# Optimization experiments

Hardware: AMD Instinct MI355X
Metric: run time of the kernel (lower is better)

The kernel has to match this reference:

```python
import jax, jax.numpy as jnp
import numpy as np

B = 64      # num graphs
NPG = 800   # nodes per graph
N = B * NPG
EPG = 6400  # edges per graph (avg degree 8)
APG = 64    # feasible actions per graph
H = 4       # attention heads
C = 64      # hidden channels per head
OUT = 128   # out_channels


def _gat_params(key, fin, h, c, concat):
    k1, k2, k3 = jax.random.split(key, 3)
    s = 1.0 / np.sqrt(fin)
    W = jax.random.uniform(k1, (fin, h * c), jnp.float32, -s, s)
    a_src = jax.random.uniform(k2, (h, c), jnp.float32, -s, s)
    a_dst = jax.random.uniform(k3, (h, c), jnp.float32, -s, s)
    b = jnp.zeros((h * c if concat else c,), jnp.float32)
    return W, a_src, a_dst, b


def _lin_params(key, fin, fout):
    k1, k2 = jax.random.split(key)
    s = 1.0 / np.sqrt(fin)
    W = jax.random.uniform(k1, (fin, fout), jnp.float32, -s, s)
    b = jax.random.uniform(k2, (fout,), jnp.float32, -s, s)
    return W, b


def setup_inputs() -> dict:
    key = jax.random.key(0)
    ks = list(jax.random.split(key, 24))
    x = jax.random.normal(ks[0], (N, 5), jnp.float32)
    offs = jnp.arange(B, dtype=jnp.int32) * NPG
    src = jax.random.randint(ks[1], (B, EPG), 0, NPG, jnp.int32) + offs[:, None]
    dst = jax.random.randint(ks[2], (B, EPG), 0, NPG, jnp.int32) + offs[:, None]
    edge_index = jnp.stack([src.reshape(-1), dst.reshape(-1)])
    batch = jnp.repeat(jnp.arange(B, dtype=jnp.int32), NPG)
    actions_idx = (jax.random.randint(ks[3], (B, APG, 2), 0, NPG, jnp.int32)
                   + offs[:, None, None]).reshape(-1, 2)
    tabu_label = (jax.random.uniform(ks[4], (B * APG, 1)) < 0.5).astype(jnp.float32)
    inp = dict(x=x, edge_index=edge_index, batch=batch,
               actions_idx=actions_idx, tabu_label=tabu_label)
    names = ['f1', 'f2', 'f3', 'b1', 'b2', 'b3']
    fins = [3, H * C, H * C, 3, H * C, H * C]
    hs = [H, H, 1, H, H, 1]
    cs = [C, C, OUT, C, C, OUT]
    concats = [True, True, False, True, True, False]
    for i, nm in enumerate(names):
        W, a_s, a_d, b = _gat_params(ks[5 + i], fins[i], hs[i], cs[i], concats[i])
        inp[nm + '_W'] = W; inp[nm + '_as'] = a_s; inp[nm + '_ad'] = a_d; inp[nm + '_b'] = b
    dims = [(8 * OUT + 1, 2 * OUT), (2 * OUT, 2 * OUT), (2 * OUT, 2 * OUT), (2 * OUT, 1)]
    for i, (fi, fo) in enumerate(dims):
        W, b = _lin_params(ks[12 + i], fi, fo)
        inp['p_W%d' % (i + 1)] = W; inp['p_b%d' % (i + 1)] = b
    return inp


def _gat(h, s, d, W, a_src, a_dst, bias, concat):
    # PyG GATConv: project, per-edge attention, softmax over target index, scatter-add
    n = h.shape[0]
    Hh, Cc = a_src.shape
    xp = (h @ W).reshape(n, Hh, Cc)                      # [N,H,C]
    al_s = (xp * a_src).sum(-1)                          # [N,H]
    al_d = (xp * a_dst).sum(-1)                          # [N,H]
    e = jax.nn.leaky_relu(al_s[s] + al_d[d], 0.2)        # [E,H]
    m = jax.ops.segment_max(e, d, num_segments=n)
    ex = jnp.exp(e - m[d])
    den = jax.ops.segment_sum(ex, d, num_segments=n)
    alpha = ex / (den[d] + 1e-16)
    out = jax.ops.segment_sum(xp[s] * alpha[..., None], d, num_segments=n)  # [N,H,C]
    out = out.reshape(n, Hh * Cc) if concat else out.mean(axis=1)
    return out + bias


def reference(x, edge_index, batch, actions_idx, tabu_label,
              f1_W, f1_as, f1_ad, f1_b, f2_W, f2_as, f2_ad, f2_b,
              f3_W, f3_as, f3_ad, f3_b, b1_W, b1_as, b1_ad, b1_b,
              b2_W, b2_as, b2_ad, b2_b, b3_W, b3_as, b3_ad, b3_b,
              p_W1, p_b1, p_W2, p_b2, p_W3, p_b3, p_W4, p_b4):
    n = x.shape[0]
    ar = jnp.arange(n, dtype=edge_index.dtype)
    ei = jnp.concatenate([edge_index, jnp.stack([ar, ar])], axis=1)  # add_self_loops
    src, dst = ei[0], ei[1]
    # forward branch (flow source_to_target)
    hf = x[:, jnp.array([0, 1, 3])]
    hf = jax.nn.elu(_gat(hf, src, dst, f1_W, f1_as, f1_ad, f1_b, True))
    hf = jax.nn.elu(_gat(hf, src, dst, f2_W, f2_as, f2_ad, f2_b, True))
    hf3 = _gat(hf, src, dst, f3_W, f3_as, f3_ad, f3_b, False)
    # backward branch (flow target_to_source == reversed edges)
    hb = x[:, jnp.array([0, 2, 4])]
    hb = jax.nn.elu(_gat(hb, dst, src, b1_W, b1_as, b1_ad, b1_b, True))
    hb = jax.nn.elu(_gat(hb, dst, src, b2_W, b2_as, b2_ad, b2_b, True))
    hb3 = _gat(hb, dst, src, b3_W, b3_as, b3_ad, b3_b, False)
    h_node = jnp.concatenate([hf3, hb3], axis=-1)        # [N, 2*OUT]
    counts = jax.ops.segment_sum(jnp.ones((n,), x.dtype), batch, num_segments=B)
    g_pool = jax.ops.segment_sum(h_node, batch, num_segments=B) / counts[:, None]
    node_h = jnp.concatenate([h_node, g_pool[batch]], axis=-1)  # [N, 4*OUT]
    action_h = jnp.concatenate([node_h[actions_idx[:, 0]],
                                node_h[actions_idx[:, 1]],
                                tabu_label], axis=-1)    # [A, 8*OUT+1]
    h = jnp.tanh(action_h @ p_W1 + p_b1)
    h = jnp.tanh(h @ p_W2 + p_b2)
    h = jnp.tanh(h @ p_W3 + p_b3)
    score = (h @ p_W4 + p_b4).reshape(B, APG)
    log_prob = jax.nn.log_softmax(score, axis=-1)        # [B, APG]
    entropy = -(jnp.exp(log_prob) * log_prob).sum(-1, keepdims=True)  # [B,1]
    return (log_prob, entropy)
```

## Files before the change

### kernel.cpp

```cpp
#include <hip/hip_runtime.h>
#include <hip/hip_bf16.h>
#include <math.h>

constexpr int NN  = 51200;
constexpr int EE  = 409600;
constexpr int BB  = 64;
constexpr int APG = 64;
constexpr int NPG = 800;
constexpr int SCAN_N = 2 * NN;
constexpr int NA = BB * APG;
constexpr int KF = 1056;

typedef __bf16 bf16x8 __attribute__((ext_vector_type(8)));
typedef float f32x4 __attribute__((ext_vector_type(4)));
typedef float f32x2 __attribute__((ext_vector_type(2)));
typedef __attribute__((address_space(1))) const void g_void;
typedef __attribute__((address_space(3))) void l_void;

__device__ __forceinline__ float leaky(float x) { return fmaxf(x, 0.2f * x); }
__device__ __forceinline__ float bflo(unsigned w) { return __uint_as_float(w << 16); }
__device__ __forceinline__ float bfhi(unsigned w) { return __uint_as_float(w & 0xffff0000u); }
__device__ __forceinline__ unsigned short f2b(float x) {
  __hip_bfloat16 h = __float2bfloat16(x);
  unsigned short u;
  __builtin_memcpy(&u, &h, 2);
  return u;
}
__device__ __forceinline__ unsigned pack2(float a, float b) {
  return (unsigned)f2b(a) | ((unsigned)f2b(b) << 16);
}

__global__ void count_kernel(const int* __restrict__ ei, int* cnt) {
  int e = blockIdx.x * blockDim.x + threadIdx.x;
  if (e >= EE) return;
  int s = ei[e], d = ei[EE + e];
  atomicAdd(&cnt[d], 1);
  atomicAdd(&cnt[NN + s], 1);
}

__global__ __launch_bounds__(256) void scan1_kernel(const int* __restrict__ cnt,
                                                    int* __restrict__ rp,
                                                    int* __restrict__ bsum) {
  __shared__ int wsum[4];
  int b = blockIdx.x, t = threadIdx.x;
  int base = b * 1024 + t * 4;
  int4 v = *(const int4*)(cnt + base);
  int s = v.x + v.y + v.z + v.w;
  int lane = t & 63, wv = t >> 6;
  int incl = s;
  for (int off = 1; off < 64; off <<= 1) {
    int u = __shfl_up(incl, off);
    if (lane >= off) incl += u;
  }
  if (lane == 63) wsum[wv] = incl;
  __syncthreads();
  int woff = 0;
  for (int i = 0; i < wv; i++) woff += wsum[i];
  int excl = woff + incl - s;
  rp[base] = excl;
  rp[base + 1] = excl + v.x;
  rp[base + 2] = excl + v.x + v.y;
  rp[base + 3] = excl + v.x + v.y + v.z;
  if (t == 255) bsum[b] = woff + incl;
}

__global__ void scan2_kernel(const int* __restrict__ bsum, int* __restrict__ boff,
                             int* __restrict__ rp) {
  __shared__ int w0;
  int t = threadIdx.x;
  int v = (t < 100) ? bsum[t] : 0;
  int lane = t & 63;
  int incl = v;
  for (int off = 1; off < 64; off <<= 1) {
    int u = __shfl_up(incl, off);
    if (lane >= off) incl += u;
  }
  if (t == 63) w0 = incl;
  __syncthreads();
  int excl = incl - v + ((t >= 64) ? w0 : 0);
  if (t < 100) boff[t] = excl;
  if (t == 99) rp[SCAN_N] = excl + v;
}

__global__ __launch_bounds__(256) void scan3_kernel(int* __restrict__ rp,
                                                    const int* __restrict__ boff) {
  int b = blockIdx.x;
  int off = boff[b];
  int i = b * 1024 + threadIdx.x * 4;
  int4 v = *(int4*)(rp + i);
  v.x += off; v.y += off; v.z += off; v.w += off;
  *(int4*)(rp + i) = v;
}

__global__ void fill_kernel(const int* __restrict__ ei, const int* __restrict__ rp,
                            int* pos, int* __restrict__ col) {
  int e = blockIdx.x * blockDim.x + threadIdx.x;
  if (e >= EE) return;
  int s = ei[e], d = ei[EE + e];
  int p = atomicAdd(&pos[d], 1);
  col[rp[d] + p] = s;
  int q = atomicAdd(&pos[NN + s], 1);
  col[rp[NN + s] + q] = d;
}

__global__ __launch_bounds__(256) void precomp_kernel(const float* __restrict__ Wf,
                                                      const float* __restrict__ Wb,
                                                      const float* __restrict__ asf,
                                                      const float* __restrict__ adf,
                                                      const float* __restrict__ asb,
                                                      const float* __restrict__ adb,
                                                      float* __restrict__ wa) {
  int wave = (blockIdx.x * blockDim.x + threadIdx.x) >> 6;
  int lane = threadIdx.x & 63;
  if (wave >= 48) return;
  int dir = wave / 24, sd = (wave / 12) % 2, h = (wave / 3) % 4, c = wave % 3;
  const float* W = dir ? Wb : Wf;
  const float* a = dir ? (sd ? adb : asb) : (sd ? adf : asf);
  float v = W[c * 256 + h * 64 + lane] * a[h * 64 + lane];
  for (int off = 1; off < 64; off <<= 1) v += __shfl_xor(v, off);
  if (lane == 0) wa[wave] = v;
}

__global__ __launch_bounds__(256) void lin1_kernel(const float* __restrict__ x,
                                                   const float* __restrict__ Wf,
                                                   const float* __restrict__ Wb,
                                                   const float* __restrict__ wa,
                                                   __hip_bfloat16* __restrict__ out,
                                                   float* __restrict__ al_s,
                                                   float* __restrict__ al_d) {
  int idx = blockIdx.x * 256 + threadIdx.x;
  int n = idx >> 5, grp = idx & 31;
  int dir = (n >= NN) ? 1 : 0;
  int node = dir ? n - NN : n;
  const float* W = dir ? Wb : Wf;
  int c1 = dir ? 2 : 1, c2 = dir ? 4 : 3;
  float f0 = x[node * 5], f1 = x[node * 5 + c1], f2 = x[node * 5 + c2];
  int j0 = grp * 8;
  float v[8];
#pragma unroll
  for (int j = 0; j < 8; j++)
    v[j] = f0 * W[j0 + j] + f1 * W[256 + j0 + j] + f2 * W[512 + j0 + j];
  uint4 u;
  u.x = pack2(v[0], v[1]);
  u.y = pack2(v[2], v[3]);
  u.z = pack2(v[4], v[5]);
  u.w = pack2(v[6], v[7]);
  *(uint4*)(out + (size_t)n * 256 + j0) = u;
  if (grp < 4) {
    const float* ws = wa + dir * 24 + grp * 3;
    const float* wd = wa + dir * 24 + 12 + grp * 3;
    al_s[n * 4 + grp] = f0 * ws[0] + f1 * ws[1] + f2 * ws[2];
    al_d[n * 4 + grp] = f0 * wd[0] + f1 * wd[1] + f2 * wd[2];
  }
}

template <int HH>
__global__ __launch_bounds__(256) void alpha_kernel(const float* __restrict__ als,
                                                    const float* __restrict__ ald,
                                                    const int* __restrict__ rp,
                                                    const int* __restrict__ col,
                                                    float* __restrict__ alpha,
                                                    float* __restrict__ alpha_self) {
  int b = blockIdx.x;
  int xcd = b & 7, q = b >> 3;
  int g2 = (q / 25) * 8 + xcd;
  int d = g2 * 800 + (q % 25) * 32 + (threadIdx.x >> 3);
  int slot = threadIdx.x & 7;
  int off_row = (d >= NN) ? NN : 0;
  float ald_loc[HH], self_w[HH];
#pragma unroll
  for (int h = 0; h < HH; h++) {
    ald_loc[h] = ald[d * HH + h];
    self_w[h] = __expf(leaky(als[d * HH + h] + ald_loc[h]));
  }
  int beg = rp[d], end = rp[d + 1];
  int i0 = beg + slot;
  bool have = i0 < end;
  int s0 = col[have ? i0 : beg] + off_row;
  float sm[HH], w0[HH];
#pragma unroll
  for (int h = 0; h < HH; h++) sm[h] = 0.f;
  if (have) {
#pragma unroll
    for (int h = 0; h < HH; h++) {
      w0[h] = __expf(leaky(als[s0 * HH + h] + ald_loc[h]));
      sm[h] += w0[h];
    }
  }
  for (int i = i0 + 8; i < end; i += 8) {
    int s = col[i] + off_row;
#pragma unroll
    for (int h = 0; h < HH; h++) {
      float w = __expf(leaky(als[s * HH + h] + ald_loc[h]));
      sm[h] += w;
      alpha[(size_t)i * HH + h] = w;
    }
  }
#pragma unroll
  for (int h = 0; h < HH; h++) {
    sm[h] += __shfl_xor(sm[h], 1);
    sm[h] += __shfl_xor(sm[h], 2);
    sm[h] += __shfl_xor(sm[h], 4);
  }
  float inv[HH];
#pragma unroll
  for (int h = 0; h < HH; h++)
    inv[h] = 1.f / (sm[h] + self_w[h] + 1e-16f);
  if (have) {
#pragma unroll
    for (int h = 0; h < HH; h++) alpha[(size_t)i0 * HH + h] = w0[h] * inv[h];
  }
  for (int i = i0 + 8; i < end; i += 8)
#pragma unroll
    for (int h = 0; h < HH; h++) alpha[(size_t)i * HH + h] *= inv[h];
  if (slot == 0) {
#pragma unroll
    for (int h = 0; h < HH; h++)
      alpha_self[d * HH + h] = self_w[h] * inv[h];
  }
}

__device__ __forceinline__ f32x2 unpk(unsigned w) {
  f32x2 v;
  v.x = bflo(w);
  v.y = bfhi(w);
  return v;
}

template <int HH, int CC, int OUT_SPLIT>
__global__ __launch_bounds__(256) void spmm_kernel(const __hip_bfloat16* __restrict__ xp,
                                                   const float* __restrict__ alpha,
                                                   const float* __restrict__ alpha_self,
                                                   const int* __restrict__ rp,
                                                   const int* __restrict__ col,
                                                   const float* __restrict__ biasf,
                                                   const float* __restrict__ biasb,
                                                   __hip_bfloat16* __restrict__ out_bf,
                                                   int do_elu) {
  constexpr int HC = HH * CC;
  constexpr int RDW = HC / 2;
  constexpr int DL = RDW / 32;
  int b = blockIdx.x;
  int xcd = b & 7;
  int bq = b >> 3;
  int dreg = xcd * 12800;
  int t = threadIdx.x;
  int wv = t >> 6, lane = t & 63;
  int sub = lane & 31, halfsel = lane >> 5;
  int lbase = lane & 32;
  int off_row = (dreg >= NN) ? NN : 0;
  const float* bias = (dreg >= NN) ? biasb : biasf;
  int hsel = (HH == 4) ? (sub >> 3) : 0;
  const unsigned* xw = (const unsigned*)xp;
  float bv[2 * DL];
#pragma unroll
  for (int j = 0; j < 2 * DL; j++) bv[j] = bias[sub * 2 * DL + j];

#pragma unroll 1
  for (int it = 0; it < 4; ++it) {
    int d = dreg + it * 3200 + bq * 8 + wv * 2 + halfsel;
    int beg = rp[d];
    int deg = rp[d + 1] - beg;
    int degmax = max(deg, __shfl_xor(deg, 32));
    degmax = __builtin_amdgcn_readfirstlane(degmax);
    float aself = alpha_self[d * HH + hsel];
    f32x2 acc[DL];
    {
      const unsigned* sp = xw + (size_t)d * RDW + sub * DL;
      if constexpr (DL == 4) {
        uint4 sw = *(const uint4*)sp;
        acc[0] = aself * unpk(sw.x);
        acc[1] = aself * unpk(sw.y);
        acc[2] = aself * unpk(sw.z);
        acc[3] = aself * unpk(sw.w);
      } else {
        uint2 sw = *(const uint2*)sp;
        acc[0] = aself * unpk(sw.x);
        acc[1] = aself * unpk(sw.y);
      }
    }
    for (int c0 = 0; c0 < degmax; c0 += 8) {
      int ce = c0 + sub;
      ce = (ce < deg) ? ce : (deg > 0 ? deg - 1 : 0);
      int colv = col[beg + ce];
      colv = ((unsigned)colv < (unsigned)NN) ? colv : 0;
      colv += off_row;
      float av = 0.f;
      if constexpr (HH == 4) {
        int e = c0 + (sub >> 2);
        if (e < deg) av = alpha[(size_t)(beg + e) * 4 + (sub & 3)];
      } else {
        int e = c0 + sub;
        if (e < deg) av = alpha[beg + e];
      }
      uint4 w[8];
#pragma unroll
      for (int k = 0; k < 8; k++) {
        int s = __shfl(colv, lbase + k);
        const unsigned* p = xw + (size_t)s * RDW + sub * DL;
        if constexpr (DL == 4) {
          w[k] = *(const uint4*)p;
        } else {
          uint2 v2 = *(const uint2*)p;
          w[k].x = v2.x;
          w[k].y = v2.y;
        }
      }
#pragma unroll
      for (int k = 0; k < 8; k++) {
        float a;
        if constexpr (HH == 4) a = __shfl(av, lbase + k * 4 + hsel);
        else a = __shfl(av, lbase + k);
        acc[0] += a * unpk(w[k].x);
        acc[1] += a * unpk(w[k].y);
        if constexpr (DL == 4) {
          acc[2] += a * unpk(w[k].z);
          acc[3] += a * unpk(w[k].w);
        }
      }
    }
    float v[2 * DL];
#pragma unroll
    for (int j = 0; j < DL; j++) {
      v[2 * j] = acc[j].x + bv[2 * j];
      v[2 * j + 1] = acc[j].y + bv[2 * j + 1];
    }
    if (do_elu) {
#pragma unroll
      for (int j = 0; j < 2 * DL; j++) v[j] = v[j] > 0.f ? v[j] : (__expf(v[j]) - 1.f);
    }
    if constexpr (OUT_SPLIT) {
      int nd = (d < NN) ? d : d - NN;
      int oo = (d < NN) ? 0 : 64;
      uint2 u;
      u.x = pack2(v[0], v[1]);
      u.y = pack2(v[2], v[3]);
      *(uint2*)((unsigned*)out_bf + (size_t)nd * 128 + oo + sub * 2) = u;
    } else {
      uint4 u;
      u.x = pack2(v[0], v[1]);
      u.y = pack2(v[2], v[3]);
      u.z = pack2(v[4], v[5]);
      u.w = pack2(v[6], v[7]);
      *(uint4*)((unsigned*)out_bf + (size_t)d * RDW + sub * DL) = u;
    }
  }
}

__global__ void castW2_kernel(const float* __restrict__ W0, const float* __restrict__ W1,
                              __hip_bfloat16* __restrict__ Wt0,
                              __hip_bfloat16* __restrict__ Wt1,
                              int K, int N, int Kp) {
  int idx = blockIdx.x * 256 + threadIdx.x;
  int tot = N * Kp;
  if (idx >= 2 * tot) return;
  const float* W = (idx < tot) ? W0 : W1;
  __hip_bfloat16* Wt = (idx < tot) ? Wt0 : Wt1;
  int i = (idx < tot) ? idx : idx - tot;
  int n = i / Kp, k = i % Kp;
  Wt[i] = (k < K) ? __float2bfloat16(W[(size_t)k * N + n]) : __float2bfloat16(0.f);
}

__global__ void castW1_kernel(const float* __restrict__ W, __hip_bfloat16* __restrict__ Wt,
                              int K, int N, int Kp) {
  int idx = blockIdx.x * 256 + threadIdx.x;
  if (idx >= N * Kp) return;
  int n = idx / Kp, k = idx % Kp;
  Wt[idx] = (k < K) ? __float2bfloat16(W[(size_t)k * N + n]) : __float2bfloat16(0.f);
}

template <int EPI, int ALH, int ALCC>
__global__ __launch_bounds__(256) void gemm_mfma(const __hip_bfloat16* __restrict__ A,
                                                 const __hip_bfloat16* __restrict__ Bt0,
                                                 const __hip_bfloat16* __restrict__ Bt1,
                                                 __hip_bfloat16* __restrict__ Cb,
                                                 const float* __restrict__ bias0,
                                                 const float* __restrict__ bias1,
                                                 const float* __restrict__ asv0,
                                                 const float* __restrict__ asv1,
                                                 const float* __restrict__ adv0,
                                                 const float* __restrict__ adv1,
                                                 float* __restrict__ al_s,
                                                 float* __restrict__ al_d,
                                                 int M, int N, int K, int Mhalf) {
  __shared__ __align__(16) __hip_bfloat16 As[128 * 32];
  __shared__ __align__(16) __hip_bfloat16 Bs[128 * 32];
  int t = threadIdx.x;
  int wave = t >> 6, lane = t & 63;
  int wm = (wave >> 1) * 64, wn = (wave & 1) * 64;
  int bm = blockIdx.y * 128, bn = blockIdx.x * 128;
  bool second = bm >= Mhalf;
  const __hip_bfloat16* Bt = second ? Bt1 : Bt0;
  const float* bias = second ? bias1 : bias0;
  const float* asv = second ? asv1 : asv0;
  const float* adv = second ? adv1 : adv0;

  int r0 = t >> 2, c0 = (t & 3) * 8;
  const __hip_bfloat16* Ag0 = A + (size_t)(bm + r0) * K + c0;
  const __hip_bfloat16* Ag1 = A + (size_t)(bm + r0 + 64) * K + c0;
  const __hip_bfloat16* Bg0 = Bt + (size_t)(bn + r0) * K + c0;
  const __hip_bfloat16* Bg1 = Bt + (size_t)(bn + r0 + 64) * K + c0;
  __hip_bfloat16* Asp0 = As + t * 8;
  __hip_bfloat16* Asp1 = As + 64 * 8 * 4 + t * 8;
  __hip_bfloat16* Bsp0 = Bs + t * 8;
  __hip_bfloat16* Bsp1 = Bs + 64 * 8 * 4 + t * 8;

  f32x4 acc[4][4];
#pragma unroll
  for (int i = 0; i < 4; i++)
#pragma unroll
    for (int j = 0; j < 4; j++) acc[i][j] = (f32x4)(0.f);

  int frag_off = (lane & 15) * 32 + (lane >> 4) * 8;
  const __hip_bfloat16* Ab = As + wm * 32 + frag_off;
  const __hip_bfloat16* Bb = Bs + wn * 32 + frag_off;

  for (int k0 = 0; k0 < K; k0 += 32) {
    __syncthreads();
    __builtin_amdgcn_global_load_lds((g_void*)(Ag0 + k0), (l_void*)Asp0, 16, 0, 0);
    __builtin_amdgcn_global_load_lds((g_void*)(Ag1 + k0), (l_void*)Asp1, 16, 0, 0);
    __builtin_amdgcn_global_load_lds((g_void*)(Bg0 + k0), (l_void*)Bsp0, 16, 0, 0);
    __builtin_amdgcn_global_load_lds((g_void*)(Bg1 + k0), (l_void*)Bsp1, 16, 0, 0);
    __syncthreads();
    bf16x8 af[4], bfr[4];
#pragma unroll
    for (int i = 0; i < 4; i++) af[i] = *(const bf16x8*)(Ab + i * 16 * 32);
#pragma unroll
    for (int j = 0; j < 4; j++) bfr[j] = *(const bf16x8*)(Bb + j * 16 * 32);
#pragma unroll
    for (int i = 0; i < 4; i++)
#pragma unroll
      for (int j = 0; j < 4; j++)
        acc[i][j] = __builtin_amdgcn_mfma_f32_16x16x32_bf16(af[i], bfr[j], acc[i][j], 0, 0, 0);
  }

  int cr = (lane >> 4) * 4, cc = lane & 15;

  if constexpr (ALH > 0) {
    int head = (bn + wn) / ALCC;
    float as_c[4], ad_c[4];
#pragma unroll
    for (int j = 0; j < 4; j++) {
      int colx = bn + wn + j * 16 + cc;
      as_c[j] = asv[colx];
      ad_c[j] = adv[colx];
    }
#pragma unroll
    for (int i = 0; i < 4; i++)
#pragma unroll
      for (int r = 0; r < 4; r++) {
        float ps = 0.f, pd = 0.f;
#pragma unroll
        for (int j = 0; j < 4; j++) {
          ps += acc[i][j][r] * as_c[j];
          pd += acc[i][j][r] * ad_c[j];
        }
        ps += __shfl_xor(ps, 1); pd += __shfl_xor(pd, 1);
        ps += __shfl_xor(ps, 2); pd += __shfl_xor(pd, 2);
        ps += __shfl_xor(ps, 4); pd += __shfl_xor(pd, 4);
        ps += __shfl_xor(ps, 8); pd += __shfl_xor(pd, 8);
        if ((lane & 15) == 0) {
          int row = bm + wm + i * 16 + cr + r;
          if (ALCC > 64) {
            atomicAdd(&al_s[row * ALH + head], ps);
            atomicAdd(&al_d[row * ALH + head], pd);
          } else {
            al_s[row * ALH + head] = ps;
            al_d[row * ALH + head] = pd;
          }
        }
      }
  }

#pragma unroll
  for (int i = 0; i < 4; i++)
#pragma unroll
    for (int j = 0; j < 4; j++) {
      int colx = bn + wn + j * 16 + cc;
      float bs = (EPI == 2) ? bias[colx] : 0.f;
#pragma unroll
      for (int r = 0; r < 4; r++) {
        float v = acc[i][j][r];
        if (EPI == 2) v = tanhf(v + bs);
        Cb[(size_t)(bm + wm + i * 16 + cr + r) * N + colx] = __float2bfloat16(v);
      }
    }
}

__global__ void pool1_kernel(const __hip_bfloat16* __restrict__ h_node,
                             float* __restrict__ part) {
  int g = blockIdx.y, c = blockIdx.x, t = threadIdx.x;
  const unsigned* base = (const unsigned*)h_node + ((size_t)g * NPG + c * 100) * 128 + t;
  f32x2 s = (f32x2)(0.f);
  for (int i = 0; i < 100; i++) s += unpk(base[(size_t)i * 128]);
  part[(size_t)(g * 8 + c) * 256 + 2 * t] = s.x;
  part[(size_t)(g * 8 + c) * 256 + 2 * t + 1] = s.y;
}

__global__ void pool2_kernel(const float* __restrict__ part, float* __restrict__ g_pool) {
  int g = blockIdx.x, t = threadIdx.x;
  float s = 0.f;
  for (int c = 0; c < 8; c++) s += part[(size_t)(g * 8 + c) * 256 + t];
  g_pool[g * 256 + t] = s * (1.f / NPG);
}

__global__ __launch_bounds__(256) void buildfeat_kernel(const __hip_bfloat16* __restrict__ h_node,
                                                        const float* __restrict__ g_pool,
                                                        const int* __restrict__ actions,
                                                        const float* __restrict__ tabu,
                                                        const int* __restrict__ batch,
                                                        __hip_bfloat16* __restrict__ feat) {
  int a = (blockIdx.x * blockDim.x + threadIdx.x) >> 6;
  int lane = threadIdx.x & 63;
  if (a >= NA) return;
  int n0 = actions[a * 2], n1 = actions[a * 2 + 1];
  int g = batch[n0];
  ushort4 v0 = *(const ushort4*)(h_node + (size_t)n0 * 256 + lane * 4);
  float4 vg = *(const float4*)(g_pool + (size_t)g * 256 + lane * 4);
  ushort4 v1 = *(const ushort4*)(h_node + (size_t)n1 * 256 + lane * 4);
  __hip_bfloat16* fr = feat + (size_t)a * KF;
  ushort4 ug = make_ushort4(f2b(vg.x), f2b(vg.y), f2b(vg.z), f2b(vg.w));
  *(ushort4*)(fr + lane * 4) = v0;
  *(ushort4*)(fr + 256 + lane * 4) = ug;
  *(ushort4*)(fr + 512 + lane * 4) = v1;
  *(ushort4*)(fr + 768 + lane * 4) = ug;
  if (lane < 8) {
    float t0 = (lane == 0) ? tabu[a] : 0.f;
    ushort4 u = make_ushort4(f2b(t0), 0, 0, 0);
    *(ushort4*)(fr + 1024 + lane * 4) = u;
  }
}

__global__ __launch_bounds__(256) void head_kernel(const __hip_bfloat16* __restrict__ y,
                                                   const float* __restrict__ W4,
                                                   const float* __restrict__ b4,
                                                   float* __restrict__ out) {
  __shared__ float sc[64];
  int g = blockIdx.x;
  int t = threadIdx.x;
  int a = t >> 2, sub = t & 3;
  int aid = g * 64 + a;
  const unsigned* row = (const unsigned*)(y + (size_t)aid * 256) + sub * 32;
  const float* w = W4 + sub * 64;
  float s = 0.f;
#pragma unroll
  for (int q = 0; q < 32; q++) {
    s += bflo(row[q]) * w[2 * q] + bfhi(row[q]) * w[2 * q + 1];
  }
  s += __shfl_xor(s, 1);
  s += __shfl_xor(s, 2);
  if (sub == 0) sc[a] = s + b4[0];
  __syncthreads();
  if (t < 64) {
    float v = sc[t];
    float m = v;
    for (int off = 1; off < 64; off <<= 1) m = fmaxf(m, __shfl_xor(m, off));
    float ex = expf(v - m);
    float sum = ex;
    for (int off = 1; off < 64; off <<= 1) sum += __shfl_xor(sum, off);
    float lp = v - m - logf(sum);
    out[g * 64 + t] = lp;
    float pe = (ex / sum) * lp;
    for (int off = 1; off < 64; off <<= 1) pe += __shfl_xor(pe, off);
    if (t == 0) out[BB * APG + g] = -pe;
  }
}

extern "C" void kernel_launch(void* const* d_in, const int* in_sizes, int n_in,
                              void* d_out, int out_size, void* d_ws, size_t ws_size,
                              hipStream_t stream) {
  const float* x = (const float*)d_in[0];
  const int* ei = (const int*)d_in[1];
  const int* batch = (const int*)d_in[2];
  const int* actions = (const int*)d_in[3];
  const float* tabu = (const float*)d_in[4];
  const float* fW[3] = {(const float*)d_in[5], (const float*)d_in[9], (const float*)d_in[13]};
  const float* fas[3] = {(const float*)d_in[6], (const float*)d_in[10], (const float*)d_in[14]};
  const float* fad[3] = {(const float*)d_in[7], (const float*)d_in[11], (const float*)d_in[15]};
  const float* fb[3] = {(const float*)d_in[8], (const float*)d_in[12], (const float*)d_in[16]};
  const float* bW[3] = {(const float*)d_in[17], (const float*)d_in[21], (const float*)d_in[25]};
  const float* bas[3] = {(const float*)d_in[18], (const float*)d_in[22], (const float*)d_in[26]};
  const float* bad[3] = {(const float*)d_in[19], (const float*)d_in[23], (const float*)d_in[27]};
  const float* bb[3] = {(const float*)d_in[20], (const float*)d_in[24], (const float*)d_in[28]};
  const float* pW1 = (const float*)d_in[29];
  const float* pb1 = (const float*)d_in[30];
  const float* pW2 = (const float*)d_in[31];
  const float* pb2 = (const float*)d_in[32];
  const float* pW3 = (const float*)d_in[33];
  const float* pb3 = (const float*)d_in[34];
  const float* pW4 = (const float*)d_in[35];
  const float* pb4 = (const float*)d_in[36];
  float* out = (float*)d_out;

  char* ws = (char*)d_ws;
  size_t o = 0;
  auto alloc = [&](size_t bytes) -> void* {
    o = (o + 255) & ~(size_t)255;
    void* p = ws + o;
    o += bytes;
    return p;
  };
  int* cnt = (int*)alloc((size_t)4 * NN * 4);
  int* rp = (int*)alloc((size_t)(SCAN_N + 1) * 4);
  int* col = (int*)alloc(((size_t)2 * EE + 64) * 4);
  int* bsum = (int*)alloc(128 * 4);
  int* boff = (int*)alloc(128 * 4);
  float* al_s = (float*)alloc((size_t)SCAN_N * 4 * 4);
  float* al_d = (float*)alloc((size_t)SCAN_N * 4 * 4);
  float* alpha = (float*)alloc((size_t)2 * EE * 4 * 4);
  float* alpha_self = (float*)alloc((size_t)SCAN_N * 4 * 4);
  float* wa = (float*)alloc(64 * 4);
  __hip_bfloat16* xp = (__hip_bfloat16*)alloc((size_t)SCAN_N * 256 * 2);
  __hip_bfloat16* bufA = (__hip_bfloat16*)alloc((size_t)SCAN_N * 256 * 2);
  __hip_bfloat16* h_node = (__hip_bfloat16*)alloc((size_t)NN * 256 * 2);
  __hip_bfloat16* wt0 = (__hip_bfloat16*)alloc((size_t)256 * KF * 2);
  __hip_bfloat16* wt1 = (__hip_bfloat16*)alloc((size_t)256 * KF * 2);
  float* part = (float*)alloc((size_t)BB * 8 * 256 * 4);
  float* g_pool = (float*)alloc((size_t)BB * 256 * 4);
  __hip_bfloat16* feat = xp;
  __hip_bfloat16* y1 = feat + (size_t)NA * KF;
  __hip_bfloat16* y2 = y1 + (size_t)NA * 256;

  hipMemsetAsync(cnt, 0, (size_t)4 * NN * 4, stream);
  count_kernel<<<(EE + 255) / 256, 256, 0, stream>>>(ei, cnt);
  scan1_kernel<<<SCAN_N / 1024, 256, 0, stream>>>(cnt, rp, bsum);
  scan2_kernel<<<1, 128, 0, stream>>>(bsum, boff, rp);
  scan3_kernel<<<SCAN_N / 1024, 256, 0, stream>>>(rp, boff);
  fill_kernel<<<(EE + 255) / 256, 256, 0, stream>>>(ei, rp, cnt + 2 * NN, col);

  const int nwb = 3200;
  const int nab = SCAN_N * 8 / 256;

  precomp_kernel<<<12, 256, 0, stream>>>(fW[0], bW[0], fas[0], fad[0], bas[0], bad[0], wa);
  lin1_kernel<<<SCAN_N * 32 / 256, 256, 0, stream>>>(x, fW[0], bW[0], wa, xp, al_s, al_d);
  alpha_kernel<4><<<nab, 256, 0, stream>>>(al_s, al_d, rp, col, alpha, alpha_self);
  spmm_kernel<4, 64, 0><<<nwb, 256, 0, stream>>>(xp, alpha, alpha_self, rp, col,
                                                 fb[0], bb[0], bufA, 1);
  castW2_kernel<<<(2 * 256 * 256 + 255) / 256, 256, 0, stream>>>(fW[1], bW[1], wt0, wt1,
                                                                 256, 256, 256);
  gemm_mfma<1, 4, 64><<<dim3(2, SCAN_N / 128), 256, 0, stream>>>(
      bufA, wt0, wt1, xp, nullptr, nullptr, fas[1], bas[1], fad[1], bad[1],
      al_s, al_d, SCAN_N, 256, 256, NN);
  alpha_kernel<4><<<nab, 256, 0, stream>>>(al_s, al_d, rp, col, alpha, alpha_self);
  spmm_kernel<4, 64, 0><<<nwb, 256, 0, stream>>>(xp, alpha, alpha_self, rp, col,
                                                 fb[1], bb[1], bufA, 1);
  castW2_kernel<<<(2 * 128 * 256 + 255) / 256, 256, 0, stream>>>(fW[2], bW[2], wt0, wt1,
                                                                 256, 128, 256);
  hipMemsetAsync(al_s, 0, (size_t)2 * SCAN_N * 4, stream);
  gemm_mfma<1, 1, 128><<<dim3(1, SCAN_N / 128), 256, 0, stream>>>(
      bufA, wt0, wt1, xp, nullptr, nullptr, fas[2], bas[2], fad[2], bad[2],
      al_s, al_d, SCAN_N, 128, 256, NN);
  alpha_kernel<1><<<nab, 256, 0, stream>>>(al_s, al_d, rp, col, alpha, alpha_self);
  spmm_kernel<1, 128, 1><<<nwb, 256, 0, stream>>>(xp, alpha, alpha_self, rp, col,
                                                  fb[2], bb[2], h_node, 0);

  pool1_kernel<<<dim3(8, BB), 128, 0, stream>>>(h_node, part);
  pool2_kernel<<<BB, 256, 0, stream>>>(part, g_pool);

  buildfeat_kernel<<<NA / 4, 256, 0, stream>>>(h_node, g_pool, actions, tabu, batch, feat);
  castW1_kernel<<<(256 * KF + 255) / 256, 256, 0, stream>>>(pW1, wt0, 1025, 256, KF);
  gemm_mfma<2, 0, 64><<<dim3(2, NA / 128), 256, 0, stream>>>(
      feat, wt0, wt0, y1, pb1, pb1, nullptr, nullptr, nullptr, nullptr,
      nullptr, nullptr, NA, 256, KF, 1 << 30);
  castW2_kernel<<<(2 * 256 * 256 + 255) / 256, 256, 0, stream>>>(pW2, pW3, wt0, wt1,
                                                                 256, 256, 256);
  gemm_mfma<2, 0, 64><<<dim3(2, NA / 128), 256, 0, stream>>>(
      y1, wt0, wt0, y2, pb2, pb2, nullptr, nullptr, nullptr, nullptr,
      nullptr, nullptr, NA, 256, 256, 1 << 30);
  gemm_mfma<2, 0, 64><<<dim3(2, NA / 128), 256, 0, stream>>>(
      y2, wt1, wt1, y1, pb3, pb3, nullptr, nullptr, nullptr, nullptr,
      nullptr, nullptr, NA, 256, 256, 1 << 30);
  head_kernel<<<BB, 256, 0, stream>>>(y1, pW4, pb4, out);
}
```

Before: 506.8 us.

## Fuse attention softmax computation into SpMM aggregation kernel

Removes the separate alpha_kernel and computes the edge attention weights and their softmax normalisation inside the SpMM kernel. Column indices for the first 64 edges are held in registers and reused for both the weights and the gathers, with a slower scalar fallback for higher degrees. This removes three launches and the write and re-read of the per-edge alpha array, at the cost of more registers and exp work inside the gather-bound kernel.

New measurement: 511.7 us. About the same (+1.0%).

```diff
diff --git a/kernel.cpp b/kernel.cpp
--- a/kernel.cpp
+++ b/kernel.cpp
@@ -154,72 +154,6 @@
   }
 }
 
-template <int HH>
-__global__ __launch_bounds__(256) void alpha_kernel(const float* __restrict__ als,
-                                                    const float* __restrict__ ald,
-                                                    const int* __restrict__ rp,
-                                                    const int* __restrict__ col,
-                                                    float* __restrict__ alpha,
-                                                    float* __restrict__ alpha_self) {
-  int b = blockIdx.x;
-  int xcd = b & 7, q = b >> 3;
-  int g2 = (q / 25) * 8 + xcd;
-  int d = g2 * 800 + (q % 25) * 32 + (threadIdx.x >> 3);
-  int slot = threadIdx.x & 7;
-  int off_row = (d >= NN) ? NN : 0;
-  float ald_loc[HH], self_w[HH];
-#pragma unroll
-  for (int h = 0; h < HH; h++) {
-    ald_loc[h] = ald[d * HH + h];
-    self_w[h] = __expf(leaky(als[d * HH + h] + ald_loc[h]));
-  }
-  int beg = rp[d], end = rp[d + 1];
-  int i0 = beg + slot;
-  bool have = i0 < end;
-  int s0 = col[have ? i0 : beg] + off_row;
-  float sm[HH], w0[HH];
-#pragma unroll
-  for (int h = 0; h < HH; h++) sm[h] = 0.f;
-  if (have) {
-#pragma unroll
-    for (int h = 0; h < HH; h++) {
-      w0[h] = __expf(leaky(als[s0 * HH + h] + ald_loc[h]));
-      sm[h] += w0[h];
-    }
-  }
-  for (int i = i0 + 8; i < end; i += 8) {
-    int s = col[i] + off_row;
-#pragma unroll
-    for (int h = 0; h < HH; h++) {
-      float w = __expf(leaky(als[s * HH + h] + ald_loc[h]));
-      sm[h] += w;
-      alpha[(size_t)i * HH + h] = w;
-    }
-  }
-#pragma unroll
-  for (int h = 0; h < HH; h++) {
-    sm[h] += __shfl_xor(sm[h], 1);
-    sm[h] += __shfl_xor(sm[h], 2);
-    sm[h] += __shfl_xor(sm[h], 4);
-  }
-  float inv[HH];
-#pragma unroll
-  for (int h = 0; h < HH; h++)
-    inv[h] = 1.f / (sm[h] + self_w[h] + 1e-16f);
-  if (have) {
-#pragma unroll
-    for (int h = 0; h < HH; h++) alpha[(size_t)i0 * HH + h] = w0[h] * inv[h];
-  }
-  for (int i = i0 + 8; i < end; i += 8)
-#pragma unroll
-    for (int h = 0; h < HH; h++) alpha[(size_t)i * HH + h] *= inv[h];
-  if (slot == 0) {
-#pragma unroll
-    for (int h = 0; h < HH; h++)
-      alpha_self[d * HH + h] = self_w[h] * inv[h];
-  }
-}
-
 __device__ __forceinline__ f32x2 unpk(unsigned w) {
   f32x2 v;
   v.x = bflo(w);
@@ -229,8 +163,8 @@
 
 template <int HH, int CC, int OUT_SPLIT>
 __global__ __launch_bounds__(256) void spmm_kernel(const __hip_bfloat16* __restrict__ xp,
-                                                   const float* __restrict__ alpha,
-                                                   const float* __restrict__ alpha_self,
+                                                   const float* __restrict__ als,
+                                                   const float* __restrict__ ald,
                                                    const int* __restrict__ rp,
                                                    const int* __restrict__ col,
                                                    const float* __restrict__ biasf,
@@ -240,6 +174,7 @@
   constexpr int HC = HH * CC;
   constexpr int RDW = HC / 2;
   constexpr int DL = RDW / 32;
+  constexpr int NWQ = (HH == 4) ? 8 : 2;
   int b = blockIdx.x;
   int xcd = b & 7;
   int bq = b >> 3;
@@ -250,7 +185,8 @@
   int lbase = lane & 32;
   int off_row = (dreg >= NN) ? NN : 0;
   const float* bias = (dreg >= NN) ? biasb : biasf;
-  int hsel = (HH == 4) ? (sub >> 3) : 0;
+  int hch = (HH == 4) ? (sub >> 3) : 0;
+  int hat = (HH == 4) ? (sub & 3) : 0;
   const unsigned* xw = (const unsigned*)xp;
   float bv[2 * DL];
 #pragma unroll
@@ -263,7 +199,78 @@
     int deg = rp[d + 1] - beg;
     int degmax = max(deg, __shfl_xor(deg, 32));
     degmax = __builtin_amdgcn_readfirstlane(degmax);
-    float aself = alpha_self[d * HH + hsel];
+
+    float ald_d = ald[(size_t)d * HH + hat];
+    float als_d = als[(size_t)d * HH + hat];
+    float selfw = __expf(leaky(als_d + ald_d));
+
+    int e0 = (sub < deg) ? sub : (deg - 1);
+    e0 = (e0 < 0) ? 0 : e0;
+    int cA = col[beg + e0];
+    cA = (((unsigned)cA < (unsigned)NN) ? cA : 0) + off_row;
+    int cB = off_row;
+    if (degmax > 32) {
+      int e1 = (32 + sub < deg) ? (32 + sub) : (deg - 1);
+      e1 = (e1 < 0) ? 0 : e1;
+      cB = col[beg + e1];
+      cB = (((unsigned)cB < (unsigned)NN) ? cB : 0) + off_row;
+    }
+
+    float wq[NWQ];
+    float den = 0.f;
+    if constexpr (HH == 4) {
+#pragma unroll
+      for (int g = 0; g < 8; ++g) {
+        float w = 0.f;
+        if (g * 8 < degmax) {
+          int e = g * 8 + (sub >> 2);
+          int s = __shfl((g < 4) ? cA : cB, lbase + (g & 3) * 8 + (sub >> 2));
+          if (e < deg) w = __expf(leaky(als[(size_t)s * 4 + hat] + ald_d));
+        }
+        wq[g] = w;
+        den += w;
+      }
+      for (int e = 64; e < degmax; ++e) {
+        if (e < deg) {
+          int s = col[beg + e];
+          s = (((unsigned)s < (unsigned)NN) ? s : 0) + off_row;
+          den += __expf(leaky(als[(size_t)s * 4 + hat] + ald_d));
+        }
+      }
+      den += __shfl_xor(den, 4);
+      den += __shfl_xor(den, 8);
+      den += __shfl_xor(den, 16);
+    } else {
+#pragma unroll
+      for (int g = 0; g < 2; ++g) {
+        float w = 0.f;
+        if (g * 32 < degmax) {
+          int e = g * 32 + sub;
+          int s = g ? cB : cA;
+          if (e < deg) w = __expf(leaky(als[s] + ald_d));
+        }
+        wq[g] = w;
+        den += w;
+      }
+      for (int e = 64; e < degmax; ++e) {
+        if (e < deg) {
+          int s = col[beg + e];
+          s = (((unsigned)s < (unsigned)NN) ? s : 0) + off_row;
+          den += __expf(leaky(als[s] + ald_d));
+        }
+      }
+      den += __shfl_xor(den, 1);
+      den += __shfl_xor(den, 2);
+      den += __shfl_xor(den, 4);
+      den += __shfl_xor(den, 8);
+      den += __shfl_xor(den, 16);
+    }
+    float inv = 1.f / (den + selfw + 1e-16f);
+#pragma unroll
+    for (int g = 0; g < NWQ; ++g) wq[g] *= inv;
+    float aself = selfw * inv;
+    if constexpr (HH == 4) aself = __shfl(aself, lbase + (sub >> 3));
+
     f32x2 acc[DL];
     {
       const unsigned* sp = xw + (size_t)d * RDW + sub * DL;
@@ -279,46 +286,58 @@
         acc[1] = aself * unpk(sw.y);
       }
     }
-    for (int c0 = 0; c0 < degmax; c0 += 8) {
-      int ce = c0 + sub;
-      ce = (ce < deg) ? ce : (deg > 0 ? deg - 1 : 0);
-      int colv = col[beg + ce];
-      colv = ((unsigned)colv < (unsigned)NN) ? colv : 0;
-      colv += off_row;
-      float av = 0.f;
+#pragma unroll
+    for (int c = 0; c < 8; ++c) {
+      if (c * 8 < degmax) {
+        uint4 w8[8];
+#pragma unroll
+        for (int k = 0; k < 8; ++k) {
+          int s = __shfl((c < 4) ? cA : cB, lbase + (c & 3) * 8 + k);
+          const unsigned* p = xw + (size_t)s * RDW + sub * DL;
+          if constexpr (DL == 4) {
+            w8[k] = *(const uint4*)p;
+          } else {
+            uint2 v2 = *(const uint2*)p;
+            w8[k].x = v2.x;
+            w8[k].y = v2.y;
+          }
+        }
+#pragma unroll
+        for (int k = 0; k < 8; ++k) {
+          float a;
+          if constexpr (HH == 4) a = __shfl(wq[c], lbase + k * 4 + hch);
+          else a = __shfl(wq[c >> 2], lbase + (c & 3) * 8 + k);
+          acc[0] += a * unpk(w8[k].x);
+          acc[1] += a * unpk(w8[k].y);
+          if constexpr (DL == 4) {
+            acc[2] += a * unpk(w8[k].z);
+            acc[3] += a * unpk(w8[k].w);
+          }
+        }
+      }
+    }
+    if (degmax > 64) {
+      float invc = inv, aldc = ald_d;
       if constexpr (HH == 4) {
-        int e = c0 + (sub >> 2);
-        if (e < deg) av = alpha[(size_t)(beg + e) * 4 + (sub & 3)];
-      } else {
-        int e = c0 + sub;
-        if (e < deg) av = alpha[beg + e];
-      }
-      uint4 w[8];
-#pragma unroll
-      for (int k = 0; k < 8; k++) {
-        int s = __shfl(colv, lbase + k);
-        const unsigned* p = xw + (size_t)s * RDW + sub * DL;
-        if constexpr (DL == 4) {
-          w[k] = *(const uint4*)p;
-        } else {
-          uint2 v2 = *(const uint2*)p;
-          w[k].x = v2.x;
-          w[k].y = v2.y;
-        }
-      }
-#pragma unroll
-      for (int k = 0; k < 8; k++) {
-        float a;
-        if constexpr (HH == 4) a = __shfl(av, lbase + k * 4 + hsel);
-        else a = __shfl(av, lbase + k);
-        acc[0] += a * unpk(w[k].x);
-        acc[1] += a * unpk(w[k].y);
-        if constexpr (DL == 4) {
-          acc[2] += a * unpk(w[k].z);
-          acc[3] += a * unpk(w[k].w);
-        }
-      }
-    }
+        invc = __shfl(inv, lbase + (sub >> 3));
+        aldc = __shfl(ald_d, lbase + (sub >> 3));
+      }
+      for (int e = 64; e < degmax; ++e) {
+        if (e < deg) {
+          int s = col[beg + e];
+          s = (((unsigned)s < (unsigned)NN) ? s : 0) + off_row;
+          float a = __expf(leaky(als[(size_t)s * HH + hch] + aldc)) * invc;
+          const unsigned* p = xw + (size_t)s * RDW + sub * DL;
+          acc[0] += a * unpk(p[0]);
+          acc[1] += a * unpk(p[1]);
+          if constexpr (DL == 4) {
+            acc[2] += a * unpk(p[2]);
+            acc[3] += a * unpk(p[3]);
+          }
+        }
+      }
+    }
+
     float v[2 * DL];
 #pragma unroll
     for (int j = 0; j < DL; j++) {
@@ -607,9 +626,6 @@
   int* boff = (int*)alloc(128 * 4);
   float* al_s = (float*)alloc((size_t)SCAN_N * 4 * 4);
   float* al_d = (float*)alloc((size_t)SCAN_N * 4 * 4);
-  float* alpha = (float*)alloc((size_t)2 * EE * 4 * 4);
-  float* alpha_self = (float*)alloc((size_t)SCAN_N * 4 * 4);
-  float* wa = (float*)alloc(64 * 4);
   __hip_bfloat16* xp = (__hip_bfloat16*)alloc((size_t)SCAN_N * 256 * 2);
   __hip_bfloat16* bufA = (__hip_bfloat16*)alloc((size_t)SCAN_N * 256 * 2);
   __hip_bfloat16* h_node = (__hip_bfloat16*)alloc((size_t)NN * 256 * 2);
@@ -617,6 +633,7 @@
   __hip_bfloat16* wt1 = (__hip_bfloat16*)alloc((size_t)256 * KF * 2);
   float* part = (float*)alloc((size_t)BB * 8 * 256 * 4);
   float* g_pool = (float*)alloc((size_t)BB * 256 * 4);
+  float* wa = (float*)alloc(64 * 4);
   __hip_bfloat16* feat = xp;
   __hip_bfloat16* y1 = feat + (size_t)NA * KF;
   __hip_bfloat16* y2 = y1 + (size_t)NA * 256;
@@ -629,20 +646,17 @@
   fill_kernel<<<(EE + 255) / 256, 256, 0, stream>>>(ei, rp, cnt + 2 * NN, col);
 
   const int nwb = 3200;
-  const int nab = SCAN_N * 8 / 256;
 
   precomp_kernel<<<12, 256, 0, stream>>>(fW[0], bW[0], fas[0], fad[0], bas[0], bad[0], wa);
   lin1_kernel<<<SCAN_N * 32 / 256, 256, 0, stream>>>(x, fW[0], bW[0], wa, xp, al_s, al_d);
-  alpha_kernel<4><<<nab, 256, 0, stream>>>(al_s, al_d, rp, col, alpha, alpha_self);
-  spmm_kernel<4, 64, 0><<<nwb, 256, 0, stream>>>(xp, alpha, alpha_self, rp, col,
+  spmm_kernel<4, 64, 0><<<nwb, 256, 0, stream>>>(xp, al_s, al_d, rp, col,
                                                  fb[0], bb[0], bufA, 1);
   castW2_kernel<<<(2 * 256 * 256 + 255) / 256, 256, 0, stream>>>(fW[1], bW[1], wt0, wt1,
                                                                  256, 256, 256);
   gemm_mfma<1, 4, 64><<<dim3(2, SCAN_N / 128), 256, 0, stream>>>(
       bufA, wt0, wt1, xp, nullptr, nullptr, fas[1], bas[1], fad[1], bad[1],
       al_s, al_d, SCAN_N, 256, 256, NN);
-  alpha_kernel<4><<<nab, 256, 0, stream>>>(al_s, al_d, rp, col, alpha, alpha_self);
-  spmm_kernel<4, 64, 0><<<nwb, 256, 0, stream>>>(xp, alpha, alpha_self, rp, col,
+  spmm_kernel<4, 64, 0><<<nwb, 256, 0, stream>>>(xp, al_s, al_d, rp, col,
                                                  fb[1], bb[1], bufA, 1);
   castW2_kernel<<<(2 * 128 * 256 + 255) / 256, 256, 0, stream>>>(fW[2], bW[2], wt0, wt1,
                                                                  256, 128, 256);
@@ -650,8 +664,7 @@
   gemm_mfma<1, 1, 128><<<dim3(1, SCAN_N / 128), 256, 0, stream>>>(
       bufA, wt0, wt1, xp, nullptr, nullptr, fas[2], bas[2], fad[2], bad[2],
       al_s, al_d, SCAN_N, 128, 256, NN);
-  alpha_kernel<1><<<nab, 256, 0, stream>>>(al_s, al_d, rp, col, alpha, alpha_self);
-  spmm_kernel<1, 128, 1><<<nwb, 256, 0, stream>>>(xp, alpha, alpha_self, rp, col,
+  spmm_kernel<1, 128, 1><<<nwb, 256, 0, stream>>>(xp, al_s, al_d, rp, col,
                                                   fb[2], bb[2], h_node, 0);
 
   pool1_kernel<<<dim3(8, BB), 128, 0, stream>>>(h_node, part);
```
